# Performance work log

Measured on AMD Instinct MI355X. Metric: run time of the kernel, lower is better.

## Reference

```python
import jax, jax.numpy as jnp
import numpy as np

NS, BS, U, NR, NT, D = 256, 7, 8, 4, 8, 2
ITERS, HID = 3, 200
P, NOISE = 100.0, 1e-7
CIN = 2 * NT * D  # block input width: flattened Z1 and Z2


def setup_inputs() -> dict:
    key = jax.random.key(0)
    ks = jax.random.split(key, 21)
    rn = lambda k, s: jax.random.normal(k, s, dtype=jnp.float32)
    inp = {
        'H_re': rn(ks[0], (NS, BS, BS, U, NR, NT)),
        'H_im': rn(ks[1], (NS, BS, BS, U, NR, NT)),
        'V_re': rn(ks[2], (NS, BS, U, NT, D)),
        'V_im': rn(ks[3], (NS, BS, U, NT, D)),
        'w': jnp.ones((U,), jnp.float32),
        'W1_re': rn(ks[4], (ITERS, HID, CIN)) * 0.05,
        'W1_im': rn(ks[5], (ITERS, HID, CIN)) * 0.05,
        'b1_re': rn(ks[6], (ITERS, HID)) * 0.05,
        'b1_im': rn(ks[7], (ITERS, HID)) * 0.05,
        'W2_re': rn(ks[8], (ITERS, HID, HID)) * 0.05,
        'W2_im': rn(ks[9], (ITERS, HID, HID)) * 0.05,
        'b2_re': rn(ks[10], (ITERS, HID)) * 0.05,
        'b2_im': rn(ks[11], (ITERS, HID)) * 0.05,
        'W3_re': rn(ks[12], (ITERS, HID, HID)) * 0.05,
        'W3_im': rn(ks[13], (ITERS, HID, HID)) * 0.05,
        'b3_re': rn(ks[14], (ITERS, HID)) * 0.05,
        'b3_im': rn(ks[15], (ITERS, HID)) * 0.05,
        'W4_re': rn(ks[16], (ITERS, 1, HID)) * 0.05,
        'W4_im': rn(ks[17], (ITERS, 1, HID)) * 0.05,
        'b4_re': rn(ks[18], (ITERS, 1)) * 0.05,
        'b4_im': rn(ks[19], (ITERS, 1)) * 0.05,
    }
    return inp


def _crelu(x):
    # ComplexReLU: relu on real part, imaginary part passes through
    return jax.nn.relu(x.real) + 1j * x.imag


def _clin(x, W, b):
    # torch Linear with complex weights: x @ W.T + b
    return jnp.einsum('...i,oi->...o', x, W) + b


def _iteration(H, V, w, p):
    n = H.shape[0]
    Z = V
    # HV[n,k,l,i,j] = H[n,k,l,i] @ V[n,k,j]  -> [n,BS,BS,U,U,NR,D]
    HV = jnp.einsum('nklirt,nkjtd->nklijrd', H, V)
    ab = jnp.arange(BS)
    au = jnp.arange(U)
    HV2 = HV[:, ab, ab][:, :, au, au]  # HV[:,k,k,i,i] -> [n,BS,U,NR,D]
    # T[n,k,l,i,j] = HV @ HV^H -> [n,BS,BS,U,U,NR,NR]
    T = jnp.einsum('nklijrd,nklijsd->nklijrs', HV, HV.conj())
    I_r = jnp.eye(NR, dtype=HV.dtype)
    # U[n,l,u] = noise*I + sum_{k,j} T[n,k,l,u,j]
    Usum = NOISE * I_r + T.sum(axis=(1, 4))  # [n,BS,U,NR,NR]
    Y = jnp.linalg.solve(Usum, HV2)
    Td = T[:, ab, ab][:, :, au, au]  # T[:,l,l,u,u]
    F = Usum - Td
    Gamma = jnp.einsum('nlurd,nlure->nlude', HV2.conj(), jnp.linalg.solve(F, HV2))
    IG = jnp.eye(D, dtype=HV.dtype) + Gamma  # [n,BS,U,D,D]
    # A[n,l,m,u] = H[n,l,m,u].mH @ Y[n,m,u] -> [n,BS,BS,U,NT,D]
    A = jnp.einsum('nlmurt,nmurd->nlmutd', H.conj(), Y)
    # L[n,l,u] = sum_m A @ IG[m,u] @ A^H -> [n,BS,U,NT,NT]
    L = jnp.einsum('nlmutd,nmude,nlmuse->nluts', A, IG, A.conj())
    All = A[:, ab, ab]  # A[:,l,l] -> [n,BS,U,NT,D]
    Lam = jnp.einsum('nlutd,nlude->nlute', All, IG)
    wv = w.astype(HV.dtype)[None, None, :, None, None]
    Lam = Lam * wv
    L = L * wv
    Z2 = Lam - jnp.einsum('nluts,nlusd->nlutd', L, Z)
    inp = jnp.concatenate([Z.reshape(n, BS, U, NT * D), Z2.reshape(n, BS, U, NT * D)], -1)
    W1, b1, W2, b2, W3, b3, W4, b4 = p
    h = _crelu(_clin(inp, W1, b1))
    h = _crelu(_clin(h, W2, b2))
    h = _crelu(_clin(h, W3, b3))
    step = _clin(h, W4, b4).real  # [n,BS,U,1]
    Vn = Z + step[..., None] * Z2
    fro = (jnp.abs(Vn) ** 2).sum((-2, -1)).sum(2)  # [n,BS]
    scale = jnp.where(fro > P, jnp.sqrt(P / fro), 1.0)
    return Vn * scale[:, :, None, None, None].astype(Vn.dtype)


def reference(H_re, H_im, V_re, V_im, w, W1_re, W1_im, b1_re, b1_im, W2_re, W2_im, b2_re, b2_im, W3_re, W3_im, b3_re, b3_im, W4_re, W4_im, b4_re, b4_im):
    H = (H_re + 1j * H_im).astype(jnp.complex64)
    V = (V_re + 1j * V_im).astype(jnp.complex64)
    # init_input power normalization per (sample, BS)
    fro0 = (jnp.abs(V) ** 2).sum((-2, -1)).sum(2)
    V = V * jnp.sqrt(P / fro0)[:, :, None, None, None].astype(V.dtype)
    c64 = jnp.complex64
    Ws = [(W1_re + 1j * W1_im).astype(c64), (b1_re + 1j * b1_im).astype(c64),
          (W2_re + 1j * W2_im).astype(c64), (b2_re + 1j * b2_im).astype(c64),
          (W3_re + 1j * W3_im).astype(c64), (b3_re + 1j * b3_im).astype(c64),
          (W4_re + 1j * W4_im).astype(c64), (b4_re + 1j * b4_im).astype(c64)]
    for it in range(ITERS):
        p = tuple(a[it] for a in Ws)
        V = _iteration(H, V, w, p)
    return jnp.stack([V.real, V.imag], axis=-1)
```

## Files before the change

kernel.cpp:

```cpp
#include <hip/hip_runtime.h>
#include <math.h>

#define NS 256
#define BS 7
#define UU 8
#define NR 4
#define NT 8
#define DD 2
#define HID 200
#define CIN 32
#define PP 100.0f
#define NOISEF 1e-7f

typedef _Float16 f16x8 __attribute__((ext_vector_type(8)));
typedef float f32x4 __attribute__((ext_vector_type(4)));

#define AST 424
#define AST0 104
#define NTILES 28
#define B1_KC 3
#define B23_KC 13
#define B1_HALVES (B1_KC*NTILES*64*8)
#define B23_HALVES (B23_KC*NTILES*64*8)
#define BITER_HALVES (B1_HALVES + 2*B23_HALVES)
#define MROWS 32

__device__ void chol_solve(const float2 (*A)[NR], const float2 (*B)[DD], float2 (*X)[DD]) {
  float2 L[NR][NR];
  for (int j = 0; j < NR; ++j) {
    float d = A[j][j].x;
    for (int k = 0; k < j; ++k) d -= L[j][k].x * L[j][k].x + L[j][k].y * L[j][k].y;
    float ld = sqrtf(fmaxf(d, 1e-30f));
    L[j][j] = make_float2(ld, 0.f);
    float inv = 1.f / ld;
    for (int i = j + 1; i < NR; ++i) {
      float sr = A[i][j].x, si = A[i][j].y;
      for (int k = 0; k < j; ++k) {
        float2 a = L[i][k], b = L[j][k];
        sr -= a.x * b.x + a.y * b.y;
        si -= a.y * b.x - a.x * b.y;
      }
      L[i][j] = make_float2(sr * inv, si * inv);
    }
  }
  for (int c = 0; c < DD; ++c) {
    float2 z[NR];
    for (int i = 0; i < NR; ++i) {
      float sr = B[i][c].x, si = B[i][c].y;
      for (int k = 0; k < i; ++k) {
        float2 a = L[i][k], zz = z[k];
        sr -= a.x * zz.x - a.y * zz.y;
        si -= a.x * zz.y + a.y * zz.x;
      }
      float inv = 1.f / L[i][i].x;
      z[i] = make_float2(sr * inv, si * inv);
    }
    for (int i = NR - 1; i >= 0; --i) {
      float sr = z[i].x, si = z[i].y;
      for (int k = i + 1; k < NR; ++k) {
        float2 a = L[k][i], xx = X[k][c];
        sr -= a.x * xx.x + a.y * xx.y;
        si -= a.x * xx.y - a.y * xx.x;
      }
      float inv = 1.f / L[i][i].x;
      X[i][c] = make_float2(sr * inv, si * inv);
    }
  }
}

__global__ void k_norm0(const float* __restrict__ Vre, const float* __restrict__ Vim,
                        float2* __restrict__ Vcur) {
  int nl = blockIdx.x;
  int tid = threadIdx.x;
  size_t base = (size_t)nl * 128;
  float re = Vre[base + tid], im = Vim[base + tid];
  float p = re * re + im * im;
  p += __shfl_down(p, 32); p += __shfl_down(p, 16); p += __shfl_down(p, 8);
  p += __shfl_down(p, 4);  p += __shfl_down(p, 2);  p += __shfl_down(p, 1);
  __shared__ float sred[2];
  if ((tid & 63) == 0) sred[tid >> 6] = p;
  __syncthreads();
  float fro = sred[0] + sred[1];
  float sc = sqrtf(PP / fro);
  Vcur[base + tid] = make_float2(re * sc, im * sc);
}

__global__ __launch_bounds__(448) void k_C(const float2* __restrict__ Vcur,
    float2* __restrict__ Cb) {
  int n = blockIdx.x;
  int tid = threadIdx.x;
  __shared__ float2 Vs[952];
  const float2* Vn = Vcur + (size_t)n * 896;
  for (int idx = tid; idx < 896; idx += 448)
    Vs[(idx >> 4) * 17 + (idx & 15)] = Vn[idx];
  __syncthreads();
  int k = tid >> 6, e = tid & 63, c = e >> 3, t = e & 7;
  float sr = 0.f, si = 0.f;
  #pragma unroll
  for (int j = 0; j < 8; ++j) {
    const float2* vr = &Vs[(k * 8 + j) * 17];
    #pragma unroll
    for (int d = 0; d < 2; ++d) {
      float2 a = vr[t * 2 + d], b = vr[c * 2 + d];
      sr += a.x * b.x + a.y * b.y;
      si += a.y * b.x - a.x * b.y;
    }
  }
  Cb[((size_t)(n * 7 + k) * 8 + c) * 8 + t] = make_float2(sr, si);
}

__global__ __launch_bounds__(64) void k_gpart(const float* __restrict__ Hre,
    const float* __restrict__ Him, const float2* __restrict__ Vcur,
    const float2* __restrict__ Cb, float2* __restrict__ Gpart,
    float2* __restrict__ Tdb, float2* __restrict__ HV2b) {
  int blk = blockIdx.x;
  int k = blk % 7; int l = (blk / 7) % 7; int n = blk / 49;
  int lane = threadIdx.x;
  int i = lane >> 3, c = lane & 7;
  size_t b_nli = (size_t)n * 56 + l * 8 + i;

  __shared__ float2 Hs[8 * 33];
  __shared__ float2 Cs[8 * 9];

  {
    size_t hbase = ((size_t)(n * 7 + k) * 7 + l) * 256;
    int idx = lane * 4;
    float4 re = *(const float4*)(Hre + hbase + idx);
    float4 im = *(const float4*)(Him + hbase + idx);
    int ii = idx >> 5, rem = idx & 31;
    float2* hp = &Hs[ii * 33 + rem];
    hp[0] = make_float2(re.x, im.x);
    hp[1] = make_float2(re.y, im.y);
    hp[2] = make_float2(re.z, im.z);
    hp[3] = make_float2(re.w, im.w);
  }
  if (lane < 32) {
    const float* cp = (const float*)(Cb + (size_t)(n * 7 + k) * 64);
    float4 vv = *(const float4*)(cp + lane * 4);
    int e0 = lane * 2;
    Cs[(e0 >> 3) * 9 + (e0 & 7)]       = make_float2(vv.x, vv.y);
    Cs[((e0 + 1) >> 3) * 9 + ((e0 + 1) & 7)] = make_float2(vv.z, vv.w);
  }
  __syncthreads();

  const float2* hme = &Hs[i * 33];
  const float2* cme = &Cs[c * 9];

  float2 T[4];
  #pragma unroll
  for (int r = 0; r < 4; ++r) {
    float tr = 0.f, ti = 0.f;
    #pragma unroll
    for (int t = 0; t < 8; ++t) {
      float2 h = hme[r * 8 + t], cc = cme[t];
      tr += h.x * cc.x - h.y * cc.y;
      ti += h.x * cc.y + h.y * cc.x;
    }
    T[r] = make_float2(tr, ti);
  }
  float2 G[10];
  {
    int ui = 0;
    #pragma unroll
    for (int r = 0; r < 4; ++r)
      #pragma unroll
      for (int s = r; s < 4; ++s) {
        float2 a = T[r], hb = hme[s * 8 + c];
        G[ui].x = a.x * hb.x + a.y * hb.y;
        G[ui].y = a.y * hb.x - a.x * hb.y;
        ++ui;
      }
  }
  #pragma unroll
  for (int m = 1; m < 8; m <<= 1) {
    #pragma unroll
    for (int q = 0; q < 10; ++q) {
      G[q].x += __shfl_xor(G[q].x, m);
      G[q].y += __shfl_xor(G[q].y, m);
    }
  }
  if (c == 0) {
    float2* gp = Gpart + (b_nli * 7 + k) * 10;
    #pragma unroll
    for (int q = 0; q < 10; ++q) gp[q] = G[q];
  }

  if (k == l) {
    const float2* vp = Vcur + b_nli * 16;
    float2 v[8][2];
    #pragma unroll
    for (int q = 0; q < 8; ++q) {
      float4 vv = *(const float4*)(vp + 2 * q);
      v[q][0] = make_float2(vv.x, vv.y);
      v[q][1] = make_float2(vv.z, vv.w);
    }
    float2 hv[4][2];
    #pragma unroll
    for (int r = 0; r < 4; ++r)
      #pragma unroll
      for (int d = 0; d < 2; ++d) {
        float ar = 0.f, ai = 0.f;
        #pragma unroll
        for (int t = 0; t < 8; ++t) {
          float2 h = hme[r * 8 + t];
          ar += h.x * v[t][d].x - h.y * v[t][d].y;
          ai += h.x * v[t][d].y + h.y * v[t][d].x;
        }
        hv[r][d] = make_float2(ar, ai);
      }
    if (c == 0) {
      float2* tdp = Tdb + b_nli * 10;
      int ui = 0;
      #pragma unroll
      for (int r = 0; r < 4; ++r)
        #pragma unroll
        for (int s = r; s < 4; ++s) {
          float tr = 0.f, ti = 0.f;
          #pragma unroll
          for (int d = 0; d < 2; ++d) {
            float2 a = hv[r][d], cx = hv[s][d];
            tr += a.x * cx.x + a.y * cx.y;
            ti += a.y * cx.x - a.x * cx.y;
          }
          tdp[ui] = make_float2(tr, ti);
          ++ui;
        }
      float2* h2p = HV2b + b_nli * 8;
      #pragma unroll
      for (int x = 0; x < 8; ++x) h2p[x] = hv[x >> 1][x & 1];
    }
  }
}

__global__ __launch_bounds__(256) void k_solveR(const float2* __restrict__ Gpart,
    const float2* __restrict__ Tdb, const float2* __restrict__ HV2b,
    float2* __restrict__ Yb, float2* __restrict__ IGb) {
  int gid = blockIdx.x * 256 + threadIdx.x;
  int which = (gid >= 14336) ? 1 : 0;
  int b = gid - which * 14336;

  float2 G[10];
  #pragma unroll
  for (int q = 0; q < 10; ++q) G[q] = make_float2(0.f, 0.f);
  const float2* gp = Gpart + (size_t)b * 70;
  #pragma unroll
  for (int k = 0; k < 7; ++k)
    #pragma unroll
    for (int q = 0; q < 10; ++q) {
      float2 g = gp[k * 10 + q];
      G[q].x += g.x; G[q].y += g.y;
    }
  if (which) {
    const float2* tp = Tdb + (size_t)b * 10;
    #pragma unroll
    for (int q = 0; q < 10; ++q) { float2 t = tp[q]; G[q].x -= t.x; G[q].y -= t.y; }
  }
  float2 M[NR][NR];
  {
    int ui = 0;
    #pragma unroll
    for (int r = 0; r < 4; ++r)
      #pragma unroll
      for (int s = r; s < 4; ++s) {
        M[r][s] = G[ui];
        M[s][r] = make_float2(G[ui].x, -G[ui].y);
        ++ui;
      }
    #pragma unroll
    for (int r = 0; r < 4; ++r) { M[r][r].x += NOISEF; M[r][r].y = 0.f; }
  }
  float2 Bv[NR][DD], X[NR][DD];
  const float2* hp = HV2b + (size_t)b * 8;
  #pragma unroll
  for (int x = 0; x < 8; ++x) Bv[x >> 1][x & 1] = hp[x];
  chol_solve(M, Bv, X);
  if (!which) {
    #pragma unroll
    for (int x = 0; x < 8; ++x) Yb[(size_t)b * 8 + x] = X[x >> 1][x & 1];
  } else {
    #pragma unroll
    for (int d = 0; d < DD; ++d)
      #pragma unroll
      for (int e = 0; e < DD; ++e) {
        float gr = (d == e) ? 1.f : 0.f, gi = 0.f;
        #pragma unroll
        for (int r = 0; r < NR; ++r) {
          float2 a = Bv[r][d], x = X[r][e];
          gr += a.x * x.x + a.y * x.y;
          gi += a.x * x.y - a.y * x.x;
        }
        IGb[(size_t)b * 4 + d * 2 + e] = make_float2(gr, gi);
      }
  }
}

__global__ __launch_bounds__(256) void k_stage2(const float* __restrict__ Hre,
    const float* __restrict__ Him, const float2* __restrict__ Vcur,
    const float2* __restrict__ Yb, const float2* __restrict__ IGb,
    const float* __restrict__ w, float2* __restrict__ Z2out) {
  int nl = blockIdx.x; int l = nl % BS; int n = nl / BS;
  int tid = threadIdx.x;
  __shared__ float2 SM[3686];
  float2* Hsm  = SM;
  float2* Bsm  = SM;
  float2* Lsm  = SM + 952;
  float2* Ysm  = SM + 1792;
  float2* IGsm = SM + 2247;
  float2* Asm  = SM + 2478;
  float2* Lamm = SM + 3430;
  float2* Zlm  = SM + 3558;

  size_t hbase = ((size_t)n * BS + l) * 1792;
  for (int idx = tid; idx < 1792; idx += 256) {
    int t = idx & 7, r = (idx >> 3) & 3, u = (idx >> 5) & 7, m = idx >> 8;
    Hsm[((u * 4 + r) * 7 + m) * 8 + t] = make_float2(Hre[hbase + idx], Him[hbase + idx]);
  }
  const float2* yp = Yb + (size_t)n * 448;
  for (int idx = tid; idx < 448; idx += 256)
    Ysm[(idx >> 6) * 65 + (idx & 63)] = yp[idx];
  const float2* igp = IGb + (size_t)n * 224;
  if (tid < 224) IGsm[(tid >> 5) * 33 + (tid & 31)] = igp[tid];
  const float2* zp = Vcur + (size_t)nl * 128;
  if (tid < 128) Zlm[tid] = zp[tid];
  __syncthreads();

  for (int idx = tid; idx < 896; idx += 256) {
    int u = idx / 112, rem = idx % 112, m = rem >> 4, t = (rem >> 1) & 7, d = rem & 1;
    float ar = 0.f, ai = 0.f;
    #pragma unroll
    for (int r = 0; r < NR; ++r) {
      float2 h = Hsm[((u * 4 + r) * 7 + m) * 8 + t];
      float2 y = Ysm[m * 65 + u * 8 + r * 2 + d];
      ar += h.x * y.x + h.y * y.y;
      ai += h.x * y.y - h.y * y.x;
    }
    Asm[u * 119 + m * 17 + t * 2 + d] = make_float2(ar, ai);
  }
  __syncthreads();

  for (int idx = tid; idx < 896; idx += 256) {
    int u = idx / 112, rem = idx % 112, m = rem >> 4, t = (rem >> 1) & 7, e = rem & 1;
    float br = 0.f, bi = 0.f;
    #pragma unroll
    for (int d = 0; d < DD; ++d) {
      float2 a = Asm[u * 119 + m * 17 + t * 2 + d];
      float2 g = IGsm[m * 33 + u * 4 + d * 2 + e];
      br += a.x * g.x - a.y * g.y;
      bi += a.x * g.y + a.y * g.x;
    }
    Bsm[u * 119 + m * 17 + t * 2 + e] = make_float2(br, bi);
  }
  __syncthreads();

  for (int idx = tid; idx < 512; idx += 256) {
    int u = idx >> 6, t = (idx >> 3) & 7, s = idx & 7;
    float lr = 0.f, li = 0.f;
    #pragma unroll
    for (int m = 0; m < BS; ++m)
      #pragma unroll
      for (int e = 0; e < DD; ++e) {
        float2 bb = Bsm[u * 119 + m * 17 + t * 2 + e];
        float2 ac = Asm[u * 119 + m * 17 + s * 2 + e];
        lr += bb.x * ac.x + bb.y * ac.y;
        li += bb.y * ac.x - bb.x * ac.y;
      }
    float wu = w[u];
    Lsm[(u * 8 + t) * 8 + s] = make_float2(lr * wu, li * wu);
  }
  if (tid < 128) {
    int u = tid >> 4, t = (tid >> 1) & 7, e = tid & 1;
    float ar = 0.f, ai = 0.f;
    #pragma unroll
    for (int d = 0; d < DD; ++d) {
      float2 a = Asm[u * 119 + l * 17 + t * 2 + d];
      float2 g = IGsm[l * 33 + u * 4 + d * 2 + e];
      ar += a.x * g.x - a.y * g.y;
      ai += a.x * g.y + a.y * g.x;
    }
    float wu = w[u];
    Lamm[u * 16 + t * 2 + e] = make_float2(ar * wu, ai * wu);
  }
  __syncthreads();

  if (tid < 128) {
    int u = tid >> 4, t = (tid >> 1) & 7, d = tid & 1;
    float2 lam = Lamm[u * 16 + t * 2 + d];
    float zr = lam.x, zi = lam.y;
    #pragma unroll
    for (int s = 0; s < NT; ++s) {
      float2 Lts = Lsm[(u * 8 + t) * 8 + s];
      float2 z = Zlm[u * 16 + s * 2 + d];
      zr -= Lts.x * z.x - Lts.y * z.y;
      zi -= Lts.x * z.y + Lts.y * z.x;
    }
    Z2out[(size_t)nl * 128 + u * 16 + t * 2 + d] = make_float2(zr, zi);
  }
}

__global__ __launch_bounds__(256) void k_pack(
    const float* __restrict__ W1re, const float* __restrict__ W1im,
    const float* __restrict__ b1re, const float* __restrict__ b1im,
    const float* __restrict__ W2re, const float* __restrict__ W2im,
    const float* __restrict__ b2re, const float* __restrict__ b2im,
    const float* __restrict__ W3re, const float* __restrict__ W3im,
    const float* __restrict__ b3re, const float* __restrict__ b3im,
    _Float16* __restrict__ Bout) {
  int gid = blockIdx.x * 256 + threadIdx.x;
  int lane = gid & 63;
  int rest = gid >> 6;
  int nt = rest % NTILES;
  int id2 = rest / NTILES;
  if (id2 >= 87) return;
  int iter = id2 / 29, kk = id2 % 29;
  int layer, kc;
  if (kk < 3)       { layer = 0; kc = kk; }
  else if (kk < 16) { layer = 1; kc = kk - 3; }
  else              { layer = 2; kc = kk - 16; }
  const float *Wr, *Wi, *br, *bi;
  if (layer == 0) { Wr = W1re + iter*HID*CIN; Wi = W1im + iter*HID*CIN; br = b1re + iter*HID; bi = b1im + iter*HID; }
  else if (layer == 1) { Wr = W2re + iter*HID*HID; Wi = W2im + iter*HID*HID; br = b2re + iter*HID; bi = b2im + iter*HID; }
  else { Wr = W3re + iter*HID*HID; Wi = W3im + iter*HID*HID; br = b3re + iter*HID; bi = b3im + iter*HID; }
  int c = nt * 16 + (lane & 15);
  int o = c >> 1; int odd = c & 1;
  f16x8 frag;
  #pragma unroll
  for (int j = 0; j < 8; ++j) {
    int k = kc * 32 + (lane >> 4) * 8 + j;
    float v = 0.f;
    if (o < HID) {
      if (layer == 0) {
        if (k < 32)       v = odd ? Wi[o*32 + k] : Wr[o*32 + k];
        else if (k < 64)  { int i = k - 32; v = odd ? Wr[o*32 + i] : -Wi[o*32 + i]; }
        else if (k == 64) v = odd ? bi[o] : br[o];
      } else {
        if (k < 200)       v = odd ? Wi[o*200 + k] : Wr[o*200 + k];
        else if (k == 207) v = odd ? bi[o] : br[o];
        else if (k >= 208 && k < 408) { int i = k - 208; v = odd ? Wr[o*200 + i] : -Wi[o*200 + i]; }
      }
    }
    frag[j] = (_Float16)v;
  }
  size_t off = (size_t)iter * BITER_HALVES
             + (layer == 0 ? 0 : (layer == 1 ? B1_HALVES : (B1_HALVES + B23_HALVES)))
             + ((size_t)(kc * NTILES + nt) * 64 + lane) * 8;
  *(f16x8*)(Bout + off) = frag;
}

template<int ASTRIDE, int KC, int NTL>
__device__ inline void do_gemm(const _Float16* Ain,
                               const _Float16* __restrict__ Bg,
                               _Float16* Aout, int tbase, int lane) {
  f32x4 acc[2][NTL];
  #pragma unroll
  for (int rt = 0; rt < 2; ++rt)
    #pragma unroll
    for (int nt = 0; nt < NTL; ++nt)
      acc[rt][nt] = (f32x4){0.f, 0.f, 0.f, 0.f};
  const int r0 = lane & 15, g = lane >> 4;
  const _Float16* bp0 = Bg + ((size_t)tbase * 64 + lane) * 8;
  const size_t KSTEP = (size_t)NTILES * 512;
  #pragma unroll
  for (int kc = 0; kc < KC; ++kc) {
    f16x8 b[NTL], a[2];
    #pragma unroll
    for (int nt = 0; nt < NTL; ++nt)
      b[nt] = *(const f16x8*)(bp0 + (size_t)kc * KSTEP + nt * 512);
    #pragma unroll
    for (int rt = 0; rt < 2; ++rt)
      a[rt] = *(const f16x8*)(Ain + (r0 + rt * 16) * ASTRIDE + kc * 32 + 8 * g);
    #pragma unroll
    for (int nt = 0; nt < NTL; ++nt)
      #pragma unroll
      for (int rt = 0; rt < 2; ++rt)
        acc[rt][nt] = __builtin_amdgcn_mfma_f32_16x16x32_f16(a[rt], b[nt], acc[rt][nt], 0, 0, 0);
  }
  #pragma unroll
  for (int nt = 0; nt < NTL; ++nt) {
    int c = (tbase + nt) * 16 + r0;
    int o = c >> 1;
    bool isre = !(c & 1);
    if (o < HID) {
      _Float16* outp = Aout + (isre ? o : 208 + o);
      #pragma unroll
      for (int rt = 0; rt < 2; ++rt)
        #pragma unroll
        for (int q = 0; q < 4; ++q) {
          float v = acc[rt][nt][q];
          if (isre) v = fmaxf(v, 0.f);
          outp[(size_t)(rt * 16 + g * 4 + q) * AST] = (_Float16)v;
        }
    }
  }
}

__global__ __launch_bounds__(512, 2) void k_mlp_mfma(
    const float2* __restrict__ Vcur, const float2* __restrict__ Z2,
    const _Float16* __restrict__ Bp,
    const float* __restrict__ W4re, const float* __restrict__ W4im,
    const float* __restrict__ b4re,
    float2* __restrict__ Vout) {
  int b = blockIdx.x;
  int tid = threadIdx.x;
  int wave = tid >> 6, lane = tid & 63;
  int tb = (wave < 4) ? wave * 4 : 16 + (wave - 4) * 3;

  __shared__ _Float16 A0[MROWS * AST0];
  __shared__ _Float16 Abuf[2][MROWS * AST];
  __shared__ float2 Zs[MROWS][16];
  __shared__ float2 Z2s[MROWS][16];
  __shared__ float w4s[2][HID];
  __shared__ float stepv[MROWS];
  __shared__ float scs[4];

  for (int idx = tid; idx < MROWS * 16; idx += 512) {
    ((float2*)Zs)[idx]  = Vcur[(size_t)b * (MROWS * 16) + idx];
    ((float2*)Z2s)[idx] = Z2[(size_t)b * (MROWS * 16) + idx];
  }
  for (int idx = tid; idx < HID; idx += 512) {
    w4s[0][idx] = W4re[idx];
    w4s[1][idx] = W4im[idx];
  }
  __syncthreads();

  for (int idx = tid; idx < MROWS * AST0; idx += 512) {
    int m = idx / AST0, c = idx % AST0;
    float v;
    if (c < 64) {
      int f = c & 31;
      float2 z = (f < 16) ? Zs[m][f] : Z2s[m][f - 16];
      v = (c >= 32) ? z.y : z.x;
    } else v = (c == 64) ? 1.f : 0.f;
    A0[m * AST0 + c] = (_Float16)v;
  }
  for (int idx = tid; idx < 2 * MROWS * 16; idx += 512) {
    int buf = idx >> 9, rem = idx & 511, m = rem >> 4, p = rem & 15;
    int c = (p < 8) ? (200 + p) : (400 + p);
    Abuf[buf][m * AST + c] = (p == 7) ? (_Float16)1.f : (_Float16)0.f;
  }
  __syncthreads();

  if (wave < 4) do_gemm<AST0, B1_KC, 4>(A0, Bp, &Abuf[0][0], tb, lane);
  else          do_gemm<AST0, B1_KC, 3>(A0, Bp, &Abuf[0][0], tb, lane);
  __syncthreads();
  if (wave < 4) do_gemm<AST, B23_KC, 4>(&Abuf[0][0], Bp + B1_HALVES, &Abuf[1][0], tb, lane);
  else          do_gemm<AST, B23_KC, 3>(&Abuf[0][0], Bp + B1_HALVES, &Abuf[1][0], tb, lane);
  __syncthreads();
  if (wave < 4) do_gemm<AST, B23_KC, 4>(&Abuf[1][0], Bp + B1_HALVES + B23_HALVES, &Abuf[0][0], tb, lane);
  else          do_gemm<AST, B23_KC, 3>(&Abuf[1][0], Bp + B1_HALVES + B23_HALVES, &Abuf[0][0], tb, lane);
  __syncthreads();

  {
    int m = tid >> 4, q = tid & 15;
    float acc = 0.f;
    for (int o = q; o < HID; o += 16) {
      float hr = (float)Abuf[0][m * AST + o];
      float hi = (float)Abuf[0][m * AST + 208 + o];
      acc += hr * w4s[0][o] - hi * w4s[1][o];
    }
    acc += __shfl_down(acc, 8, 16);
    acc += __shfl_down(acc, 4, 16);
    acc += __shfl_down(acc, 2, 16);
    acc += __shfl_down(acc, 1, 16);
    if (q == 0) stepv[m] = acc + b4re[0];
  }
  __syncthreads();

  {
    int idx = tid;
    int m = idx >> 4, f = idx & 15;
    float st = stepv[m];
    float2 z = Zs[m][f], z2 = Z2s[m][f];
    Zs[m][f] = make_float2(fmaf(st, z2.x, z.x), fmaf(st, z2.y, z.y));
  }
  __syncthreads();

  if (wave < 4) {
    const float2* vp = &Zs[wave * 8][0];
    float2 v0 = vp[lane * 2], v1 = vp[lane * 2 + 1];
    float p = v0.x * v0.x + v0.y * v0.y + v1.x * v1.x + v1.y * v1.y;
    p += __shfl_down(p, 32); p += __shfl_down(p, 16); p += __shfl_down(p, 8);
    p += __shfl_down(p, 4);  p += __shfl_down(p, 2);  p += __shfl_down(p, 1);
    if (lane == 0) scs[wave] = (p > PP) ? sqrtf(PP / p) : 1.f;
  }
  __syncthreads();
  {
    int idx = tid;
    float sc = scs[idx >> 7];
    float2 v = ((float2*)Zs)[idx];
    Vout[(size_t)b * (MROWS * 16) + idx] = make_float2(v.x * sc, v.y * sc);
  }
}

extern "C" void kernel_launch(void* const* d_in, const int* in_sizes, int n_in,
                              void* d_out, int out_size, void* d_ws, size_t ws_size,
                              hipStream_t stream) {
  const float* Hre  = (const float*)d_in[0];
  const float* Him  = (const float*)d_in[1];
  const float* Vre  = (const float*)d_in[2];
  const float* Vim  = (const float*)d_in[3];
  const float* w    = (const float*)d_in[4];
  const float* W1re = (const float*)d_in[5];
  const float* W1im = (const float*)d_in[6];
  const float* b1re = (const float*)d_in[7];
  const float* b1im = (const float*)d_in[8];
  const float* W2re = (const float*)d_in[9];
  const float* W2im = (const float*)d_in[10];
  const float* b2re = (const float*)d_in[11];
  const float* b2im = (const float*)d_in[12];
  const float* W3re = (const float*)d_in[13];
  const float* W3im = (const float*)d_in[14];
  const float* b3re = (const float*)d_in[15];
  const float* b3im = (const float*)d_in[16];
  const float* W4re = (const float*)d_in[17];
  const float* W4im = (const float*)d_in[18];
  const float* b4re = (const float*)d_in[19];

  const size_t NV = (size_t)NS * BS * UU * NT * DD;
  const size_t NB = (size_t)NS * BS * UU;
  float2* Vcur = (float2*)d_ws;
  float2* Z2b  = Vcur + NV;
  float2* Yb   = Z2b + NV;
  float2* IGb  = Yb + NB * 8;
  float2* Cb   = IGb + NB * 4;
  float2* Gpart= Cb + (size_t)NS * 7 * 64;
  float2* Tdb  = Gpart + NB * 70;
  float2* HV2b = Tdb + NB * 10;
  _Float16* Bpack = (_Float16*)(HV2b + NB * 8);

  k_pack<<<609, 256, 0, stream>>>(W1re, W1im, b1re, b1im, W2re, W2im, b2re, b2im,
                                  W3re, W3im, b3re, b3im, Bpack);
  k_norm0<<<NS * BS, 128, 0, stream>>>(Vre, Vim, Vcur);
  for (int it = 0; it < 3; ++it) {
    k_C<<<NS, 448, 0, stream>>>(Vcur, Cb);
    k_gpart<<<NS * BS * BS, 64, 0, stream>>>(Hre, Him, Vcur, Cb, Gpart, Tdb, HV2b);
    k_solveR<<<112, 256, 0, stream>>>(Gpart, Tdb, HV2b, Yb, IGb);
    k_stage2<<<NS * BS, 256, 0, stream>>>(Hre, Him, Vcur, Yb, IGb, w, Z2b);
    float2* vout = (it == 2) ? (float2*)d_out : Vcur;
    k_mlp_mfma<<<NS * BS * UU * NT * DD / (MROWS * 16), 512, 0, stream>>>(Vcur, Z2b,
        Bpack + (size_t)it * BITER_HALVES,
        W4re + it * HID, W4im + it * HID, b4re + it, vout);
  }
}
```

Before: 223.2 us.

## Fuse C, G-partial and Cholesky-solve kernels into one per-sample kernel

```diff
diff --git a/kernel.cpp b/kernel.cpp
--- a/kernel.cpp
+++ b/kernel.cpp
@@ -85,212 +85,201 @@
   Vcur[base + tid] = make_float2(re * sc, im * sc);
 }
 
-__global__ __launch_bounds__(448) void k_C(const float2* __restrict__ Vcur,
-    float2* __restrict__ Cb) {
+__global__ __launch_bounds__(512, 2) void k_s1n(const float* __restrict__ Hre,
+    const float* __restrict__ Him, const float2* __restrict__ Vcur,
+    float2* __restrict__ Yb, float2* __restrict__ IGb) {
   int n = blockIdx.x;
   int tid = threadIdx.x;
+  int wave = tid >> 6;
+  int lane = tid & 63;
+  int i = lane >> 3, c = lane & 7;
+
   __shared__ float2 Vs[952];
+  __shared__ float2 Cs[7][76];
+  __shared__ float2 Hl[7][268];
+  __shared__ float2 Gk[7][8][10];
+  __shared__ float2 Gs[56][10];
+  __shared__ float2 TdL[56][10];
+  __shared__ float2 HV2L[56][8];
+
   const float2* Vn = Vcur + (size_t)n * 896;
-  for (int idx = tid; idx < 896; idx += 448)
+  for (int idx = tid; idx < 896; idx += 512)
     Vs[(idx >> 4) * 17 + (idx & 15)] = Vn[idx];
   __syncthreads();
-  int k = tid >> 6, e = tid & 63, c = e >> 3, t = e & 7;
-  float sr = 0.f, si = 0.f;
-  #pragma unroll
-  for (int j = 0; j < 8; ++j) {
-    const float2* vr = &Vs[(k * 8 + j) * 17];
-    #pragma unroll
-    for (int d = 0; d < 2; ++d) {
-      float2 a = vr[t * 2 + d], b = vr[c * 2 + d];
-      sr += a.x * b.x + a.y * b.y;
-      si += a.y * b.x - a.x * b.y;
-    }
-  }
-  Cb[((size_t)(n * 7 + k) * 8 + c) * 8 + t] = make_float2(sr, si);
-}
-
-__global__ __launch_bounds__(64) void k_gpart(const float* __restrict__ Hre,
-    const float* __restrict__ Him, const float2* __restrict__ Vcur,
-    const float2* __restrict__ Cb, float2* __restrict__ Gpart,
-    float2* __restrict__ Tdb, float2* __restrict__ HV2b) {
-  int blk = blockIdx.x;
-  int k = blk % 7; int l = (blk / 7) % 7; int n = blk / 49;
-  int lane = threadIdx.x;
-  int i = lane >> 3, c = lane & 7;
-  size_t b_nli = (size_t)n * 56 + l * 8 + i;
-
-  __shared__ float2 Hs[8 * 33];
-  __shared__ float2 Cs[8 * 9];
-
-  {
-    size_t hbase = ((size_t)(n * 7 + k) * 7 + l) * 256;
-    int idx = lane * 4;
-    float4 re = *(const float4*)(Hre + hbase + idx);
-    float4 im = *(const float4*)(Him + hbase + idx);
-    int ii = idx >> 5, rem = idx & 31;
-    float2* hp = &Hs[ii * 33 + rem];
-    hp[0] = make_float2(re.x, im.x);
-    hp[1] = make_float2(re.y, im.y);
-    hp[2] = make_float2(re.z, im.z);
-    hp[3] = make_float2(re.w, im.w);
-  }
-  if (lane < 32) {
-    const float* cp = (const float*)(Cb + (size_t)(n * 7 + k) * 64);
-    float4 vv = *(const float4*)(cp + lane * 4);
-    int e0 = lane * 2;
-    Cs[(e0 >> 3) * 9 + (e0 & 7)]       = make_float2(vv.x, vv.y);
-    Cs[((e0 + 1) >> 3) * 9 + ((e0 + 1) & 7)] = make_float2(vv.z, vv.w);
-  }
-  __syncthreads();
-
-  const float2* hme = &Hs[i * 33];
-  const float2* cme = &Cs[c * 9];
-
-  float2 T[4];
-  #pragma unroll
-  for (int r = 0; r < 4; ++r) {
-    float tr = 0.f, ti = 0.f;
-    #pragma unroll
-    for (int t = 0; t < 8; ++t) {
-      float2 h = hme[r * 8 + t], cc = cme[t];
-      tr += h.x * cc.x - h.y * cc.y;
-      ti += h.x * cc.y + h.y * cc.x;
-    }
-    T[r] = make_float2(tr, ti);
-  }
-  float2 G[10];
-  {
-    int ui = 0;
-    #pragma unroll
-    for (int r = 0; r < 4; ++r)
-      #pragma unroll
-      for (int s = r; s < 4; ++s) {
-        float2 a = T[r], hb = hme[s * 8 + c];
-        G[ui].x = a.x * hb.x + a.y * hb.y;
-        G[ui].y = a.y * hb.x - a.x * hb.y;
-        ++ui;
-      }
-  }
-  #pragma unroll
-  for (int m = 1; m < 8; m <<= 1) {
-    #pragma unroll
-    for (int q = 0; q < 10; ++q) {
-      G[q].x += __shfl_xor(G[q].x, m);
-      G[q].y += __shfl_xor(G[q].y, m);
-    }
-  }
-  if (c == 0) {
-    float2* gp = Gpart + (b_nli * 7 + k) * 10;
-    #pragma unroll
-    for (int q = 0; q < 10; ++q) gp[q] = G[q];
-  }
-
-  if (k == l) {
-    const float2* vp = Vcur + b_nli * 16;
-    float2 v[8][2];
-    #pragma unroll
-    for (int q = 0; q < 8; ++q) {
-      float4 vv = *(const float4*)(vp + 2 * q);
-      v[q][0] = make_float2(vv.x, vv.y);
-      v[q][1] = make_float2(vv.z, vv.w);
-    }
-    float2 hv[4][2];
-    #pragma unroll
-    for (int r = 0; r < 4; ++r)
+
+  if (tid < 448) {
+    int k = tid >> 6, e = tid & 63, cc = e >> 3, t = e & 7;
+    float sr = 0.f, si = 0.f;
+    #pragma unroll
+    for (int j = 0; j < 8; ++j) {
+      const float2* vr = &Vs[(k * 8 + j) * 17];
       #pragma unroll
       for (int d = 0; d < 2; ++d) {
-        float ar = 0.f, ai = 0.f;
+        float2 a = vr[t * 2 + d], b = vr[cc * 2 + d];
+        sr += a.x * b.x + a.y * b.y;
+        si += a.y * b.x - a.x * b.y;
+      }
+    }
+    Cs[k][cc * 9 + t] = make_float2(sr, si);
+  }
+
+  for (int l = 0; l < BS; ++l) {
+    __syncthreads();
+    if (tid < 448) {
+      int k = tid >> 6;
+      int e4 = (tid & 63) * 4;
+      size_t hbase = (((size_t)(n * 7 + k) * 7) + l) * 256 + e4;
+      float4 re = *(const float4*)(Hre + hbase);
+      float4 im = *(const float4*)(Him + hbase);
+      int ii = e4 >> 5, rem = e4 & 31;
+      float2* hp = &Hl[k][ii * 33 + rem];
+      hp[0] = make_float2(re.x, im.x);
+      hp[1] = make_float2(re.y, im.y);
+      hp[2] = make_float2(re.z, im.z);
+      hp[3] = make_float2(re.w, im.w);
+    }
+    __syncthreads();
+
+    if (wave < 7) {
+      int k = wave;
+      const float2* hme = &Hl[k][i * 33];
+      const float2* cme = &Cs[k][c * 9];
+      float2 T[4];
+      #pragma unroll
+      for (int r = 0; r < 4; ++r) {
+        float tr = 0.f, ti = 0.f;
         #pragma unroll
         for (int t = 0; t < 8; ++t) {
-          float2 h = hme[r * 8 + t];
-          ar += h.x * v[t][d].x - h.y * v[t][d].y;
-          ai += h.x * v[t][d].y + h.y * v[t][d].x;
+          float2 h = hme[r * 8 + t], cv = cme[t];
+          tr += h.x * cv.x - h.y * cv.y;
+          ti += h.x * cv.y + h.y * cv.x;
         }
-        hv[r][d] = make_float2(ar, ai);
-      }
-    if (c == 0) {
-      float2* tdp = Tdb + b_nli * 10;
+        T[r] = make_float2(tr, ti);
+      }
+      float2 hb[4];
+      #pragma unroll
+      for (int s = 0; s < 4; ++s) hb[s] = hme[s * 8 + c];
+      float2 G[10];
+      {
+        int ui = 0;
+        #pragma unroll
+        for (int r = 0; r < 4; ++r)
+          #pragma unroll
+          for (int s = r; s < 4; ++s) {
+            G[ui].x = T[r].x * hb[s].x + T[r].y * hb[s].y;
+            G[ui].y = T[r].y * hb[s].x - T[r].x * hb[s].y;
+            ++ui;
+          }
+      }
+      #pragma unroll
+      for (int m = 1; m < 8; m <<= 1) {
+        #pragma unroll
+        for (int q = 0; q < 10; ++q) {
+          G[q].x += __shfl_xor(G[q].x, m);
+          G[q].y += __shfl_xor(G[q].y, m);
+        }
+      }
+      if (c == 0) {
+        #pragma unroll
+        for (int q = 0; q < 10; ++q) Gk[k][i][q] = G[q];
+      }
+
+      if (k == l) {
+        int r = c >> 1, d = c & 1;
+        float hvx = 0.f, hvy = 0.f;
+        const float2* vp = &Vs[(l * 8 + i) * 17 + d];
+        #pragma unroll
+        for (int t = 0; t < 8; ++t) {
+          float2 h = hme[r * 8 + t], v = vp[t * 2];
+          hvx += h.x * v.x - h.y * v.y;
+          hvy += h.x * v.y + h.y * v.x;
+        }
+        float gx[8], gy[8];
+        int base = lane & 56;
+        #pragma unroll
+        for (int p = 0; p < 8; ++p) {
+          gx[p] = __shfl(hvx, base + p);
+          gy[p] = __shfl(hvy, base + p);
+        }
+        if (c == 0) {
+          int ui = 0;
+          #pragma unroll
+          for (int r2 = 0; r2 < 4; ++r2)
+            #pragma unroll
+            for (int s2 = r2; s2 < 4; ++s2) {
+              float tr = 0.f, ti = 0.f;
+              #pragma unroll
+              for (int d2 = 0; d2 < 2; ++d2) {
+                float ax = gx[r2 * 2 + d2], ay = gy[r2 * 2 + d2];
+                float bx = gx[s2 * 2 + d2], by = gy[s2 * 2 + d2];
+                tr += ax * bx + ay * by;
+                ti += ay * bx - ax * by;
+              }
+              TdL[l * 8 + i][ui] = make_float2(tr, ti);
+              ++ui;
+            }
+          #pragma unroll
+          for (int x = 0; x < 8; ++x)
+            HV2L[l * 8 + i][x] = make_float2(gx[x], gy[x]);
+        }
+      }
+    }
+    __syncthreads();
+    if (tid < 80) {
+      int ii = tid / 10, q = tid % 10;
+      float sx = 0.f, sy = 0.f;
+      #pragma unroll
+      for (int k = 0; k < 7; ++k) {
+        float2 g = Gk[k][ii][q];
+        sx += g.x; sy += g.y;
+      }
+      Gs[l * 8 + ii][q] = make_float2(sx, sy);
+    }
+  }
+  __syncthreads();
+
+  if (tid < 128) {
+    int which = tid >> 6;
+    int b = tid & 63;
+    if (b < 56) {
+      float2 M[NR][NR];
       int ui = 0;
       #pragma unroll
       for (int r = 0; r < 4; ++r)
         #pragma unroll
         for (int s = r; s < 4; ++s) {
-          float tr = 0.f, ti = 0.f;
+          float2 g = Gs[b][ui];
+          if (which) { float2 td = TdL[b][ui]; g.x -= td.x; g.y -= td.y; }
+          ++ui;
+          M[r][s] = g;
+          M[s][r] = make_float2(g.x, -g.y);
+        }
+      #pragma unroll
+      for (int r = 0; r < 4; ++r) { M[r][r].x += NOISEF; M[r][r].y = 0.f; }
+      float2 Bv[NR][DD], X[NR][DD];
+      #pragma unroll
+      for (int x = 0; x < 8; ++x) Bv[x >> 1][x & 1] = HV2L[b][x];
+      chol_solve(M, Bv, X);
+      size_t gb = (size_t)n * 56 + b;
+      if (!which) {
+        #pragma unroll
+        for (int x = 0; x < 8; ++x) Yb[gb * 8 + x] = X[x >> 1][x & 1];
+      } else {
+        #pragma unroll
+        for (int d = 0; d < DD; ++d)
           #pragma unroll
-          for (int d = 0; d < 2; ++d) {
-            float2 a = hv[r][d], cx = hv[s][d];
-            tr += a.x * cx.x + a.y * cx.y;
-            ti += a.y * cx.x - a.x * cx.y;
+          for (int e = 0; e < DD; ++e) {
+            float gr = (d == e) ? 1.f : 0.f, gi = 0.f;
+            #pragma unroll
+            for (int r = 0; r < NR; ++r) {
+              float2 a = Bv[r][d], x = X[r][e];
+              gr += a.x * x.x + a.y * x.y;
+              gi += a.x * x.y - a.y * x.x;
+            }
+            IGb[gb * 4 + d * 2 + e] = make_float2(gr, gi);
           }
-          tdp[ui] = make_float2(tr, ti);
-          ++ui;
-        }
-      float2* h2p = HV2b + b_nli * 8;
-      #pragma unroll
-      for (int x = 0; x < 8; ++x) h2p[x] = hv[x >> 1][x & 1];
-    }
-  }
-}
-
-__global__ __launch_bounds__(256) void k_solveR(const float2* __restrict__ Gpart,
-    const float2* __restrict__ Tdb, const float2* __restrict__ HV2b,
-    float2* __restrict__ Yb, float2* __restrict__ IGb) {
-  int gid = blockIdx.x * 256 + threadIdx.x;
-  int which = (gid >= 14336) ? 1 : 0;
-  int b = gid - which * 14336;
-
-  float2 G[10];
-  #pragma unroll
-  for (int q = 0; q < 10; ++q) G[q] = make_float2(0.f, 0.f);
-  const float2* gp = Gpart + (size_t)b * 70;
-  #pragma unroll
-  for (int k = 0; k < 7; ++k)
-    #pragma unroll
-    for (int q = 0; q < 10; ++q) {
-      float2 g = gp[k * 10 + q];
-      G[q].x += g.x; G[q].y += g.y;
-    }
-  if (which) {
-    const float2* tp = Tdb + (size_t)b * 10;
-    #pragma unroll
-    for (int q = 0; q < 10; ++q) { float2 t = tp[q]; G[q].x -= t.x; G[q].y -= t.y; }
-  }
-  float2 M[NR][NR];
-  {
-    int ui = 0;
-    #pragma unroll
-    for (int r = 0; r < 4; ++r)
-      #pragma unroll
-      for (int s = r; s < 4; ++s) {
-        M[r][s] = G[ui];
-        M[s][r] = make_float2(G[ui].x, -G[ui].y);
-        ++ui;
-      }
-    #pragma unroll
-    for (int r = 0; r < 4; ++r) { M[r][r].x += NOISEF; M[r][r].y = 0.f; }
-  }
-  float2 Bv[NR][DD], X[NR][DD];
-  const float2* hp = HV2b + (size_t)b * 8;
-  #pragma unroll
-  for (int x = 0; x < 8; ++x) Bv[x >> 1][x & 1] = hp[x];
-  chol_solve(M, Bv, X);
-  if (!which) {
-    #pragma unroll
-    for (int x = 0; x < 8; ++x) Yb[(size_t)b * 8 + x] = X[x >> 1][x & 1];
-  } else {
-    #pragma unroll
-    for (int d = 0; d < DD; ++d)
-      #pragma unroll
-      for (int e = 0; e < DD; ++e) {
-        float gr = (d == e) ? 1.f : 0.f, gi = 0.f;
-        #pragma unroll
-        for (int r = 0; r < NR; ++r) {
-          float2 a = Bv[r][d], x = X[r][e];
-          gr += a.x * x.x + a.y * x.y;
-          gi += a.x * x.y - a.y * x.x;
-        }
-        IGb[(size_t)b * 4 + d * 2 + e] = make_float2(gr, gi);
-      }
+      }
+    }
   }
 }
 
@@ -621,19 +610,13 @@
   float2* Z2b  = Vcur + NV;
   float2* Yb   = Z2b + NV;
   float2* IGb  = Yb + NB * 8;
-  float2* Cb   = IGb + NB * 4;
-  float2* Gpart= Cb + (size_t)NS * 7 * 64;
-  float2* Tdb  = Gpart + NB * 70;
-  float2* HV2b = Tdb + NB * 10;
-  _Float16* Bpack = (_Float16*)(HV2b + NB * 8);
+  _Float16* Bpack = (_Float16*)(IGb + NB * 4);
 
   k_pack<<<609, 256, 0, stream>>>(W1re, W1im, b1re, b1im, W2re, W2im, b2re, b2im,
                                   W3re, W3im, b3re, b3im, Bpack);
   k_norm0<<<NS * BS, 128, 0, stream>>>(Vre, Vim, Vcur);
   for (int it = 0; it < 3; ++it) {
-    k_C<<<NS, 448, 0, stream>>>(Vcur, Cb);
-    k_gpart<<<NS * BS * BS, 64, 0, stream>>>(Hre, Him, Vcur, Cb, Gpart, Tdb, HV2b);
-    k_solveR<<<112, 256, 0, stream>>>(Gpart, Tdb, HV2b, Yb, IGb);
+    k_s1n<<<NS, 512, 0, stream>>>(Hre, Him, Vcur, Yb, IGb);
     k_stage2<<<NS * BS, 256, 0, stream>>>(Hre, Him, Vcur, Yb, IGb, w, Z2b);
     float2* vout = (it == 2) ? (float2*)d_out : Vcur;
     k_mlp_mfma<<<NS * BS * UU * NT * DD / (MROWS * 16), 512, 0, stream>>>(Vcur, Z2b,
```

Result: no change. 218.9 us (-1.9%).
